# Kernel optimization log

Measured on AMD Instinct MI355X. Metric: run time of the kernel, lower is better.

Reference implementation:

```python
import jax, jax.numpy as jnp
import numpy as np

# dims: B=4 batch, S=2048 seq, D=4096 in, O=4096 out, E=16 adapters, R=16 rank

def setup_inputs() -> dict:
    key = jax.random.key(0)
    k = jax.random.split(key, 6)
    x = jax.random.normal(k[0], (4, 2048, 4096), jnp.float32)
    W = jax.random.normal(k[1], (4096, 4096), jnp.float32) * 0.02   # base_linear.weight [O, D]
    bias = jax.random.normal(k[2], (4096,), jnp.float32) * 0.02
    A = jax.random.normal(k[3], (16, 16, 4096), jnp.float32) * 0.02  # stacked a_factors [E, R, D]
    Bf = jax.random.normal(k[4], (16, 4096, 16), jnp.float32) * 0.02 # stacked b_factors [E, O, R]
    coeffs = jax.random.uniform(k[5], (16,), jnp.float32)            # task coefficients per adapter
    scales = jnp.full((16,), 0.5, jnp.float32)                       # per-adapter static scales
    return {"x": x, "W": W, "bias": bias, "A": A, "Bf": Bf, "coeffs": coeffs, "scales": scales}

def reference(x, W, bias, A, Bf, coeffs, scales):
    # base: out = x @ W.T + bias
    out = jnp.einsum('bsd,od->bso', x, W) + bias
    # fused LoRA: sum_e coeffs[e]*scales[e] * (x @ A[e].T) @ Bf[e].T
    xa = jnp.einsum('bsd,erd->ebsr', x, A)          # [E, B, S, R] (small: R=16)
    w = coeffs * scales                               # [E]
    upd = jnp.einsum('ebsr,eor,e->bso', xa, Bf, w)  # weighted accumulate over adapters
    return out + upd
```

## Files before the change

### kernel.cpp

```cpp
#include <hip/hip_runtime.h>

typedef float f32x4 __attribute__((ext_vector_type(4)));
typedef __bf16 bf16x8 __attribute__((ext_vector_type(8)));
typedef unsigned short u16x8 __attribute__((ext_vector_type(8)));

__device__ __forceinline__ unsigned short f2bf(float f) {
  union { float f; unsigned int u; } v; v.f = f;
  unsigned int u = v.u;
  unsigned int r = (u + 0x7FFFu + ((u >> 16) & 1u)) >> 16;
  return (unsigned short)r;
}

__global__ void k_cast_bf16(const float* __restrict__ in,
                            unsigned short* __restrict__ out, int n8) {
  int i = blockIdx.x * blockDim.x + threadIdx.x;
  if (i >= n8) return;
  const f32x4* p = (const f32x4*)in;
  f32x4 a = p[2 * i], b = p[2 * i + 1];
  u16x8 o;
  o[0] = f2bf(a[0]); o[1] = f2bf(a[1]); o[2] = f2bf(a[2]); o[3] = f2bf(a[3]);
  o[4] = f2bf(b[0]); o[5] = f2bf(b[1]); o[6] = f2bf(b[2]); o[7] = f2bf(b[3]);
  ((u16x8*)out)[i] = o;
}

__global__ void k_build_bw(const float* __restrict__ Bf,
                           const float* __restrict__ coeffs,
                           const float* __restrict__ scales,
                           unsigned short* __restrict__ bw) {
  int t = blockIdx.x * 256 + threadIdx.x;
  int o = t >> 8, k = t & 255, e = k >> 4, r = k & 15;
  float v = coeffs[e] * scales[e] * Bf[((size_t)e * 4096 + o) * 16 + r];
  bw[t] = f2bf(v);
}

__global__ void k_build_at(const float* __restrict__ A,
                           unsigned short* __restrict__ at) {
  __shared__ float tile[64][65];
  int kt = blockIdx.x * 64, dt = blockIdx.y * 64;
  int tx = threadIdx.x & 63, ty = threadIdx.x >> 6;
#pragma unroll
  for (int j = 0; j < 64; j += 4)
    tile[ty + j][tx] = A[(size_t)(kt + ty + j) * 4096 + dt + tx];
  __syncthreads();
#pragma unroll
  for (int j = 0; j < 64; j += 4)
    at[(size_t)(dt + ty + j) * 256 + kt + tx] = f2bf(tile[tx][ty + j]);
}

template <int M_, int N_, int K_>
__global__ __launch_bounds__(256) void k_gemm_prep(
    const unsigned short* __restrict__ Abuf,
    const unsigned short* __restrict__ Bbuf,
    const float* __restrict__ Wadd,
    unsigned short* __restrict__ outB) {
  constexpr int NBN = N_ / 128;
  constexpr int NWG = (M_ / 128) * NBN;
  const int bid = blockIdx.x;
  const int swz = (bid & 7) * (NWG / 8) + (bid >> 3);
  const int bm = swz / NBN, bn = swz % NBN;

  __shared__ unsigned short ldsA[128 * 64];
  __shared__ unsigned short ldsB[128 * 64];

  const int t = threadIdx.x, w = t >> 6, l = t & 63;
  const int wr = w >> 1, wc = w & 1;

  f32x4 acc[4][4] = {};
  const int m0 = bm * 128, n0 = bn * 128;
  const int srow = w * 8 + (l >> 3);
  const int scol = (l & 7) * 8;
  const unsigned short* gA = Abuf + (size_t)(m0 + srow) * K_ + scol;
  const unsigned short* gB = Bbuf + (size_t)(n0 + srow) * K_ + scol;

  for (int kt = 0; kt < K_; kt += 64) {
#pragma unroll
    for (int i = 0; i < 4; ++i) {
      __builtin_amdgcn_global_load_lds(
          (__attribute__((address_space(1))) void*)(gA + (size_t)i * 32 * K_ + kt),
          (__attribute__((address_space(3))) void*)(ldsA + i * 2048 + w * 512), 16, 0, 0);
      __builtin_amdgcn_global_load_lds(
          (__attribute__((address_space(1))) void*)(gB + (size_t)i * 32 * K_ + kt),
          (__attribute__((address_space(3))) void*)(ldsB + i * 2048 + w * 512), 16, 0, 0);
    }
    __syncthreads();
#pragma unroll
    for (int kk = 0; kk < 2; ++kk) {
      const int col = kk * 32 + (l >> 4) * 8;
      const int arow = wr * 64 + (l & 15);
      const int brow = wc * 64 + (l & 15);
      bf16x8 af[4], bfv[4];
#pragma unroll
      for (int mi = 0; mi < 4; ++mi)
        af[mi] = *(const bf16x8*)&ldsA[(arow + mi * 16) * 64 + col];
#pragma unroll
      for (int ni = 0; ni < 4; ++ni)
        bfv[ni] = *(const bf16x8*)&ldsB[(brow + ni * 16) * 64 + col];
#pragma unroll
      for (int mi = 0; mi < 4; ++mi)
#pragma unroll
        for (int ni = 0; ni < 4; ++ni)
          acc[mi][ni] = __builtin_amdgcn_mfma_f32_16x16x32_bf16(
              af[mi], bfv[ni], acc[mi][ni], 0, 0, 0);
    }
    __syncthreads();
  }

  const int mrow0 = m0 + wr * 64 + (l >> 4) * 4;
  const int ncol0 = n0 + wc * 64 + (l & 15);
#pragma unroll
  for (int mi = 0; mi < 4; ++mi)
#pragma unroll
    for (int r = 0; r < 4; ++r) {
      const int m = mrow0 + mi * 16 + r;
#pragma unroll
      for (int ni = 0; ni < 4; ++ni) {
        const int n = ncol0 + ni * 16;
        outB[(size_t)m * N_ + n] = f2bf(acc[mi][ni][r] + Wadd[(size_t)m * N_ + n]);
      }
    }
}

template <int M_, int N_, int K_>
__global__ __launch_bounds__(512, 2) void k_gemm256(
    const unsigned short* __restrict__ Abuf,
    const unsigned short* __restrict__ Bbuf,
    const float* __restrict__ bias,
    float* __restrict__ outF) {
  constexpr int NBN = N_ / 256;
  constexpr int NWG = (M_ / 256) * NBN;
  constexpr int NT = K_ / 32;
  static_assert(NWG % 8 == 0, "bijective xcd swizzle");
  static_assert(NT >= 4, "pipeline depth");

  const int bid = blockIdx.x;
  const int swz = (bid & 7) * (NWG / 8) + (bid >> 3);
  const int bm = swz / NBN, bn = swz % NBN;
  const int m0 = bm * 256, n0 = bn * 256;

  __shared__ __attribute__((aligned(128))) unsigned short lds[65536];
  char* ldsb = (char*)lds;

  const int tid = threadIdx.x, w = tid >> 6, l = tid & 63;
  const int wr = w >> 2, wc = w & 3;

  const int scol = ((l & 3) ^ ((l >> 3) & 3)) * 8;
  const unsigned short* gA = Abuf + (size_t)(m0 + w * 16 + (l >> 2)) * K_ + scol;
  const unsigned short* gB = Bbuf + (size_t)(n0 + w * 16 + (l >> 2)) * K_ + scol;
  const int dA = w * 1024;
  const int dB = 16384 + w * 1024;

  const int qp = ((l >> 4) ^ ((l >> 1) & 3)) * 16;
  const int raOff = (wr * 128 + (l & 15)) * 64 + qp;
  const int rbOff = 16384 + (wc * 64 + (l & 15)) * 64 + qp;

  f32x4 acc[8][4] = {};

#define STAGE_T(tt)                                                               \
  do {                                                                            \
    const int bb0_ = ((tt) & 3) << 15;                                            \
    const size_t ko_ = (size_t)(tt) * 32;                                         \
    _Pragma("unroll") for (int i_ = 0; i_ < 2; ++i_) {                            \
      __builtin_amdgcn_global_load_lds(                                           \
          (__attribute__((address_space(1))) void*)(gA + (size_t)i_ * 128 * K_ + ko_), \
          (__attribute__((address_space(3))) void*)(ldsb + bb0_ + i_ * 8192 + dA),     \
          16, 0, 0);                                                              \
      __builtin_amdgcn_global_load_lds(                                           \
          (__attribute__((address_space(1))) void*)(gB + (size_t)i_ * 128 * K_ + ko_), \
          (__attribute__((address_space(3))) void*)(ldsb + bb0_ + i_ * 8192 + dB),     \
          16, 0, 0);                                                              \
    }                                                                             \
  } while (0)

  STAGE_T(0); STAGE_T(1); STAGE_T(2);

  for (int t = 0; t < NT; ++t) {
    if (t + 2 < NT)      asm volatile("s_waitcnt vmcnt(8)" ::: "memory");
    else if (t + 1 < NT) asm volatile("s_waitcnt vmcnt(4)" ::: "memory");
    else                 asm volatile("s_waitcnt vmcnt(0)" ::: "memory");
    __builtin_amdgcn_s_barrier();

    const int bb0 = (t & 3) << 15;
    bf16x8 af[8], bv[4];
#pragma unroll
    for (int mi = 0; mi < 8; ++mi)
      af[mi] = *(const bf16x8*)(ldsb + bb0 + raOff + mi * 1024);
#pragma unroll
    for (int ni = 0; ni < 4; ++ni)
      bv[ni] = *(const bf16x8*)(ldsb + bb0 + rbOff + ni * 1024);

    if (t + 3 < NT) STAGE_T(t + 3);

    __builtin_amdgcn_s_setprio(1);
#pragma unroll
    for (int mi = 0; mi < 8; ++mi)
#pragma unroll
      for (int ni = 0; ni < 4; ++ni)
        acc[mi][ni] = __builtin_amdgcn_mfma_f32_16x16x32_bf16(
            af[mi], bv[ni], acc[mi][ni], 0, 0, 0);
    __builtin_amdgcn_s_setprio(0);
  }
#undef STAGE_T

#pragma unroll
  for (int ni = 0; ni < 4; ++ni) {
    const int n = n0 + wc * 64 + ni * 16 + (l & 15);
    const float bv2 = bias[n];
#pragma unroll
    for (int mi = 0; mi < 8; ++mi) {
      const int m = m0 + wr * 128 + mi * 16 + (l >> 4) * 4;
#pragma unroll
      for (int r = 0; r < 4; ++r)
        outF[(size_t)(m + r) * N_ + n] = acc[mi][ni][r] + bv2;
    }
  }
}

extern "C" void kernel_launch(void* const* d_in, const int* in_sizes, int n_in,
                              void* d_out, int out_size, void* d_ws, size_t ws_size,
                              hipStream_t stream) {
  const float* x      = (const float*)d_in[0];
  const float* W      = (const float*)d_in[1];
  const float* bias   = (const float*)d_in[2];
  const float* A      = (const float*)d_in[3];
  const float* Bf     = (const float*)d_in[4];
  const float* coeffs = (const float*)d_in[5];
  const float* scales = (const float*)d_in[6];
  float* out = (float*)d_out;

  char* ws = (char*)d_ws;
  unsigned short* xb   = (unsigned short*)(ws);
  unsigned short* weff = (unsigned short*)(ws + 67108864);
  unsigned short* bw   = (unsigned short*)(ws + 67108864 + 33554432);
  unsigned short* at   = (unsigned short*)(ws + 67108864 + 33554432 + 2097152);

  k_cast_bf16<<<16384, 256, 0, stream>>>(x, xb, (8192 * 4096) / 8);
  k_build_bw<<<4096, 256, 0, stream>>>(Bf, coeffs, scales, bw);
  k_build_at<<<dim3(4, 64), 256, 0, stream>>>(A, at);
  k_gemm_prep<4096, 4096, 256><<<1024, 256, 0, stream>>>(bw, at, W, weff);
  k_gemm256<8192, 4096, 4096><<<512, 512, 0, stream>>>(xb, weff, bias, out);
}
```

Before: 353.0 us.

## Switch main GEMM to 128x128 tiles with double-buffered LDS and grid-stride cast

Replaces the 256x256, 512-thread, 4-stage pipelined GEMM with a 128x128, 256-thread kernel using two LDS buffers and a barrier before each prefetch. The aim is more resident blocks per CU and lower LDS use, trading away per-tile data reuse and pipeline depth. The bf16 cast kernel is also made grid-stride with fewer blocks to cut launch overhead. The smaller tiles double global/L2 traffic per flop and add a barrier per K step.

```diff
diff --git a/kernel.cpp b/kernel.cpp
--- a/kernel.cpp
+++ b/kernel.cpp
@@ -11,16 +11,16 @@
   return (unsigned short)r;
 }
 
-__global__ void k_cast_bf16(const float* __restrict__ in,
-                            unsigned short* __restrict__ out, int n8) {
-  int i = blockIdx.x * blockDim.x + threadIdx.x;
-  if (i >= n8) return;
+__global__ __launch_bounds__(256) void k_cast_bf16(const float* __restrict__ in,
+                                                   unsigned short* __restrict__ out, int n8) {
   const f32x4* p = (const f32x4*)in;
-  f32x4 a = p[2 * i], b = p[2 * i + 1];
-  u16x8 o;
-  o[0] = f2bf(a[0]); o[1] = f2bf(a[1]); o[2] = f2bf(a[2]); o[3] = f2bf(a[3]);
-  o[4] = f2bf(b[0]); o[5] = f2bf(b[1]); o[6] = f2bf(b[2]); o[7] = f2bf(b[3]);
-  ((u16x8*)out)[i] = o;
+  for (int i = blockIdx.x * 256 + threadIdx.x; i < n8; i += 2048 * 256) {
+    f32x4 a = p[2 * i], b = p[2 * i + 1];
+    u16x8 o;
+    o[0] = f2bf(a[0]); o[1] = f2bf(a[1]); o[2] = f2bf(a[2]); o[3] = f2bf(a[3]);
+    o[4] = f2bf(b[0]); o[5] = f2bf(b[1]); o[6] = f2bf(b[2]); o[7] = f2bf(b[3]);
+    ((u16x8*)out)[i] = o;
+  }
 }
 
 __global__ void k_build_bw(const float* __restrict__ Bf,
@@ -121,83 +121,85 @@
 }
 
 template <int M_, int N_, int K_>
-__global__ __launch_bounds__(512, 2) void k_gemm256(
+__global__ __launch_bounds__(256, 4) void k_gemm128(
     const unsigned short* __restrict__ Abuf,
     const unsigned short* __restrict__ Bbuf,
     const float* __restrict__ bias,
     float* __restrict__ outF) {
-  constexpr int NBN = N_ / 256;
-  constexpr int NWG = (M_ / 256) * NBN;
+  constexpr int NBN = N_ / 128;
+  constexpr int NWG = (M_ / 128) * NBN;
   constexpr int NT = K_ / 32;
   static_assert(NWG % 8 == 0, "bijective xcd swizzle");
-  static_assert(NT >= 4, "pipeline depth");
+  static_assert(NT >= 2, "pipeline depth");
 
   const int bid = blockIdx.x;
   const int swz = (bid & 7) * (NWG / 8) + (bid >> 3);
   const int bm = swz / NBN, bn = swz % NBN;
-  const int m0 = bm * 256, n0 = bn * 256;
-
-  __shared__ __attribute__((aligned(128))) unsigned short lds[65536];
+  const int m0 = bm * 128, n0 = bn * 128;
+
+  __shared__ __attribute__((aligned(128))) unsigned short lds[16384];
   char* ldsb = (char*)lds;
 
   const int tid = threadIdx.x, w = tid >> 6, l = tid & 63;
-  const int wr = w >> 2, wc = w & 3;
+  const int wr = w >> 1, wc = w & 1;
 
   const int scol = ((l & 3) ^ ((l >> 3) & 3)) * 8;
   const unsigned short* gA = Abuf + (size_t)(m0 + w * 16 + (l >> 2)) * K_ + scol;
   const unsigned short* gB = Bbuf + (size_t)(n0 + w * 16 + (l >> 2)) * K_ + scol;
   const int dA = w * 1024;
-  const int dB = 16384 + w * 1024;
-
-  const int qp = ((l >> 4) ^ ((l >> 1) & 3)) * 16;
-  const int raOff = (wr * 128 + (l & 15)) * 64 + qp;
-  const int rbOff = 16384 + (wc * 64 + (l & 15)) * 64 + qp;
-
-  f32x4 acc[8][4] = {};
-
-#define STAGE_T(tt)                                                               \
-  do {                                                                            \
-    const int bb0_ = ((tt) & 3) << 15;                                            \
-    const size_t ko_ = (size_t)(tt) * 32;                                         \
-    _Pragma("unroll") for (int i_ = 0; i_ < 2; ++i_) {                            \
-      __builtin_amdgcn_global_load_lds(                                           \
-          (__attribute__((address_space(1))) void*)(gA + (size_t)i_ * 128 * K_ + ko_), \
-          (__attribute__((address_space(3))) void*)(ldsb + bb0_ + i_ * 8192 + dA),     \
-          16, 0, 0);                                                              \
-      __builtin_amdgcn_global_load_lds(                                           \
-          (__attribute__((address_space(1))) void*)(gB + (size_t)i_ * 128 * K_ + ko_), \
-          (__attribute__((address_space(3))) void*)(ldsb + bb0_ + i_ * 8192 + dB),     \
-          16, 0, 0);                                                              \
-    }                                                                             \
+  const int dB = 8192 + w * 1024;
+
+  const int qp = ((l >> 4) ^ ((l >> 1) & 3)) << 4;
+  const int raOff = wr * 4096 + (l & 15) * 64 + qp;
+  const int rbOff = 8192 + wc * 4096 + (l & 15) * 64 + qp;
+
+  f32x4 acc[4][4] = {};
+
+#define STAGE_T(tt)                                                                   \
+  do {                                                                                \
+    const int bb_ = ((tt) & 1) * 16384;                                               \
+    const size_t ko_ = (size_t)(tt) * 32;                                             \
+    _Pragma("unroll") for (int i_ = 0; i_ < 2; ++i_) {                                \
+      __builtin_amdgcn_global_load_lds(                                               \
+          (__attribute__((address_space(1))) void*)(gA + (size_t)i_ * 64 * K_ + ko_), \
+          (__attribute__((address_space(3))) void*)(ldsb + bb_ + i_ * 4096 + dA),     \
+          16, 0, 0);                                                                  \
+      __builtin_amdgcn_global_load_lds(                                               \
+          (__attribute__((address_space(1))) void*)(gB + (size_t)i_ * 64 * K_ + ko_), \
+          (__attribute__((address_space(3))) void*)(ldsb + bb_ + i_ * 4096 + dB),     \
+          16, 0, 0);                                                                  \
+    }                                                                                 \
   } while (0)
 
-  STAGE_T(0); STAGE_T(1); STAGE_T(2);
+  STAGE_T(0); STAGE_T(1);
 
   for (int t = 0; t < NT; ++t) {
-    if (t + 2 < NT)      asm volatile("s_waitcnt vmcnt(8)" ::: "memory");
-    else if (t + 1 < NT) asm volatile("s_waitcnt vmcnt(4)" ::: "memory");
-    else                 asm volatile("s_waitcnt vmcnt(0)" ::: "memory");
+    if (t + 1 < NT) asm volatile("s_waitcnt vmcnt(4)" ::: "memory");
+    else            asm volatile("s_waitcnt vmcnt(0)" ::: "memory");
     __builtin_amdgcn_s_barrier();
-
-    const int bb0 = (t & 3) << 15;
-    bf16x8 af[8], bv[4];
-#pragma unroll
-    for (int mi = 0; mi < 8; ++mi)
+    __builtin_amdgcn_sched_barrier(0);
+
+    const int bb0 = (t & 1) * 16384;
+    bf16x8 af[4], bv[4];
+#pragma unroll
+    for (int mi = 0; mi < 4; ++mi)
       af[mi] = *(const bf16x8*)(ldsb + bb0 + raOff + mi * 1024);
 #pragma unroll
     for (int ni = 0; ni < 4; ++ni)
       bv[ni] = *(const bf16x8*)(ldsb + bb0 + rbOff + ni * 1024);
 
-    if (t + 3 < NT) STAGE_T(t + 3);
-
     __builtin_amdgcn_s_setprio(1);
 #pragma unroll
-    for (int mi = 0; mi < 8; ++mi)
+    for (int mi = 0; mi < 4; ++mi)
 #pragma unroll
       for (int ni = 0; ni < 4; ++ni)
         acc[mi][ni] = __builtin_amdgcn_mfma_f32_16x16x32_bf16(
             af[mi], bv[ni], acc[mi][ni], 0, 0, 0);
     __builtin_amdgcn_s_setprio(0);
+
+    __builtin_amdgcn_s_barrier();
+    __builtin_amdgcn_sched_barrier(0);
+    if (t + 2 < NT) STAGE_T(t + 2);
   }
 #undef STAGE_T
 
@@ -206,8 +208,8 @@
     const int n = n0 + wc * 64 + ni * 16 + (l & 15);
     const float bv2 = bias[n];
 #pragma unroll
-    for (int mi = 0; mi < 8; ++mi) {
-      const int m = m0 + wr * 128 + mi * 16 + (l >> 4) * 4;
+    for (int mi = 0; mi < 4; ++mi) {
+      const int m = m0 + wr * 64 + mi * 16 + (l >> 4) * 4;
 #pragma unroll
       for (int r = 0; r < 4; ++r)
         outF[(size_t)(m + r) * N_ + n] = acc[mi][ni][r] + bv2;
@@ -233,9 +235,9 @@
   unsigned short* bw   = (unsigned short*)(ws + 67108864 + 33554432);
   unsigned short* at   = (unsigned short*)(ws + 67108864 + 33554432 + 2097152);
 
-  k_cast_bf16<<<16384, 256, 0, stream>>>(x, xb, (8192 * 4096) / 8);
+  k_cast_bf16<<<2048, 256, 0, stream>>>(x, xb, (8192 * 4096) / 8);
   k_build_bw<<<4096, 256, 0, stream>>>(Bf, coeffs, scales, bw);
   k_build_at<<<dim3(4, 64), 256, 0, stream>>>(A, at);
   k_gemm_prep<4096, 4096, 256><<<1024, 256, 0, stream>>>(bw, at, W, weff);
-  k_gemm256<8192, 4096, 4096><<<512, 512, 0, stream>>>(xb, weff, bias, out);
-}
+  k_gemm128<8192, 4096, 4096><<<2048, 256, 0, stream>>>(xb, weff, bias, out);
+}
```

Measured after the change: 465.9 us. 32.0% more time.

## Load GEMM B operand directly to registers and shrink LDS ring to A-only

Applied to the files above, without the earlier changes.

The main GEMM no longer stages the weight (B) operand through LDS. Each wave loads its B fragments straight into registers with inline global_load_dwordx4 into four rotating register sets. Only A goes through a 5-slot LDS ring, unrolled by four K-steps with two barriers per group instead of one per step. This cuts LDS footprint and LDS read traffic so occupancy can rise, at the cost of more VGPRs, redundant B global loads across the two wave rows, and hand-tuned vmcnt counts that are fragile. The cast kernel also becomes a grid-stride loop over 2048 blocks.

```diff
diff --git a/kernel.cpp b/kernel.cpp
--- a/kernel.cpp
+++ b/kernel.cpp
@@ -11,16 +11,16 @@
   return (unsigned short)r;
 }
 
-__global__ void k_cast_bf16(const float* __restrict__ in,
-                            unsigned short* __restrict__ out, int n8) {
-  int i = blockIdx.x * blockDim.x + threadIdx.x;
-  if (i >= n8) return;
+__global__ __launch_bounds__(256) void k_cast_bf16(const float* __restrict__ in,
+                                                   unsigned short* __restrict__ out, int n8) {
   const f32x4* p = (const f32x4*)in;
-  f32x4 a = p[2 * i], b = p[2 * i + 1];
-  u16x8 o;
-  o[0] = f2bf(a[0]); o[1] = f2bf(a[1]); o[2] = f2bf(a[2]); o[3] = f2bf(a[3]);
-  o[4] = f2bf(b[0]); o[5] = f2bf(b[1]); o[6] = f2bf(b[2]); o[7] = f2bf(b[3]);
-  ((u16x8*)out)[i] = o;
+  for (int i = blockIdx.x * 256 + threadIdx.x; i < n8; i += 2048 * 256) {
+    f32x4 a = p[2 * i], b = p[2 * i + 1];
+    u16x8 o;
+    o[0] = f2bf(a[0]); o[1] = f2bf(a[1]); o[2] = f2bf(a[2]); o[3] = f2bf(a[3]);
+    o[4] = f2bf(b[0]); o[5] = f2bf(b[1]); o[6] = f2bf(b[2]); o[7] = f2bf(b[3]);
+    ((u16x8*)out)[i] = o;
+  }
 }
 
 __global__ void k_build_bw(const float* __restrict__ Bf,
@@ -130,14 +130,14 @@
   constexpr int NWG = (M_ / 256) * NBN;
   constexpr int NT = K_ / 32;
   static_assert(NWG % 8 == 0, "bijective xcd swizzle");
-  static_assert(NT >= 4, "pipeline depth");
+  static_assert(NT % 4 == 0 && NT >= 8, "pipeline depth");
 
   const int bid = blockIdx.x;
   const int swz = (bid & 7) * (NWG / 8) + (bid >> 3);
   const int bm = swz / NBN, bn = swz % NBN;
   const int m0 = bm * 256, n0 = bn * 256;
 
-  __shared__ __attribute__((aligned(128))) unsigned short lds[65536];
+  __shared__ __attribute__((aligned(128))) unsigned short lds[40960];
   char* ldsb = (char*)lds;
 
   const int tid = threadIdx.x, w = tid >> 6, l = tid & 63;
@@ -145,61 +145,117 @@
 
   const int scol = ((l & 3) ^ ((l >> 3) & 3)) * 8;
   const unsigned short* gA = Abuf + (size_t)(m0 + w * 16 + (l >> 2)) * K_ + scol;
-  const unsigned short* gB = Bbuf + (size_t)(n0 + w * 16 + (l >> 2)) * K_ + scol;
   const int dA = w * 1024;
-  const int dB = 16384 + w * 1024;
-
-  const int qp = ((l >> 4) ^ ((l >> 1) & 3)) * 16;
+
+  const int qp = ((l >> 4) ^ ((l >> 1) & 3)) << 4;
   const int raOff = (wr * 128 + (l & 15)) * 64 + qp;
-  const int rbOff = 16384 + (wc * 64 + (l & 15)) * 64 + qp;
+
+  const unsigned long long bB0 =
+      (unsigned long long)(uintptr_t)Bbuf +
+      2ull * ((unsigned long long)(n0 + wc * 64 + (l & 15)) * K_ + ((l >> 4) * 8));
+  const unsigned long long niStep = (unsigned long long)16 * K_ * 2;
+  const unsigned long long bB1 = bB0 + niStep;
+  const unsigned long long bB2 = bB0 + 2 * niStep;
+  const unsigned long long bB3 = bB0 + 3 * niStep;
 
   f32x4 acc[8][4] = {};
-
-#define STAGE_T(tt)                                                               \
-  do {                                                                            \
-    const int bb0_ = ((tt) & 3) << 15;                                            \
-    const size_t ko_ = (size_t)(tt) * 32;                                         \
-    _Pragma("unroll") for (int i_ = 0; i_ < 2; ++i_) {                            \
-      __builtin_amdgcn_global_load_lds(                                           \
+  bf16x8 bs0[4], bs1[4], bs2[4], bs3[4];
+
+#define GLB(dst, base, toff)                                              \
+  asm volatile("global_load_dwordx4 %0, %1, off"                         \
+               : "=v"(dst)                                                \
+               : "v"((base) + (unsigned long long)(unsigned)(toff))       \
+               : "memory")
+#define LOADB(S, toff)                                                    \
+  do {                                                                    \
+    GLB(S[0], bB0, toff); GLB(S[1], bB1, toff);                           \
+    GLB(S[2], bB2, toff); GLB(S[3], bB3, toff);                           \
+  } while (0)
+
+#define STAGE_A(tt, bf)                                                                \
+  do {                                                                                 \
+    const int bb_ = (bf) * 16384;                                                      \
+    const size_t ko_ = (size_t)(tt) * 32;                                              \
+    _Pragma("unroll") for (int i_ = 0; i_ < 2; ++i_) {                                 \
+      __builtin_amdgcn_global_load_lds(                                                \
           (__attribute__((address_space(1))) void*)(gA + (size_t)i_ * 128 * K_ + ko_), \
-          (__attribute__((address_space(3))) void*)(ldsb + bb0_ + i_ * 8192 + dA),     \
-          16, 0, 0);                                                              \
-      __builtin_amdgcn_global_load_lds(                                           \
-          (__attribute__((address_space(1))) void*)(gB + (size_t)i_ * 128 * K_ + ko_), \
-          (__attribute__((address_space(3))) void*)(ldsb + bb0_ + i_ * 8192 + dB),     \
-          16, 0, 0);                                                              \
-    }                                                                             \
-  } while (0)
-
-  STAGE_T(0); STAGE_T(1); STAGE_T(2);
-
-  for (int t = 0; t < NT; ++t) {
-    if (t + 2 < NT)      asm volatile("s_waitcnt vmcnt(8)" ::: "memory");
-    else if (t + 1 < NT) asm volatile("s_waitcnt vmcnt(4)" ::: "memory");
-    else                 asm volatile("s_waitcnt vmcnt(0)" ::: "memory");
-    __builtin_amdgcn_s_barrier();
-
-    const int bb0 = (t & 3) << 15;
-    bf16x8 af[8], bv[4];
-#pragma unroll
-    for (int mi = 0; mi < 8; ++mi)
-      af[mi] = *(const bf16x8*)(ldsb + bb0 + raOff + mi * 1024);
-#pragma unroll
-    for (int ni = 0; ni < 4; ++ni)
-      bv[ni] = *(const bf16x8*)(ldsb + bb0 + rbOff + ni * 1024);
-
-    if (t + 3 < NT) STAGE_T(t + 3);
-
-    __builtin_amdgcn_s_setprio(1);
-#pragma unroll
-    for (int mi = 0; mi < 8; ++mi)
-#pragma unroll
-      for (int ni = 0; ni < 4; ++ni)
-        acc[mi][ni] = __builtin_amdgcn_mfma_f32_16x16x32_bf16(
-            af[mi], bv[ni], acc[mi][ni], 0, 0, 0);
-    __builtin_amdgcn_s_setprio(0);
-  }
-#undef STAGE_T
+          (__attribute__((address_space(3))) void*)(ldsb + bb_ + i_ * 8192 + dA),      \
+          16, 0, 0);                                                                   \
+    }                                                                                  \
+  } while (0)
+
+#define RD_A(mi, bf) (*(const bf16x8*)(ldsb + (bf) * 16384 + raOff + (mi) * 1024))
+
+#define TILE(bf, S)                                                                     \
+  do {                                                                                  \
+    bf16x8 fa0 = RD_A(0, bf), fa1 = RD_A(1, bf), fa2 = RD_A(2, bf), fa3 = RD_A(3, bf);  \
+    bf16x8 fa4 = RD_A(4, bf), fa5 = RD_A(5, bf), fa6 = RD_A(6, bf), fa7 = RD_A(7, bf);  \
+    __builtin_amdgcn_s_setprio(1);                                                      \
+    _Pragma("unroll") for (int ni_ = 0; ni_ < 4; ++ni_) {                               \
+      acc[0][ni_] = __builtin_amdgcn_mfma_f32_16x16x32_bf16(fa0, S[ni_], acc[0][ni_], 0, 0, 0); \
+      acc[1][ni_] = __builtin_amdgcn_mfma_f32_16x16x32_bf16(fa1, S[ni_], acc[1][ni_], 0, 0, 0); \
+      acc[2][ni_] = __builtin_amdgcn_mfma_f32_16x16x32_bf16(fa2, S[ni_], acc[2][ni_], 0, 0, 0); \
+      acc[3][ni_] = __builtin_amdgcn_mfma_f32_16x16x32_bf16(fa3, S[ni_], acc[3][ni_], 0, 0, 0); \
+      acc[4][ni_] = __builtin_amdgcn_mfma_f32_16x16x32_bf16(fa4, S[ni_], acc[4][ni_], 0, 0, 0); \
+      acc[5][ni_] = __builtin_amdgcn_mfma_f32_16x16x32_bf16(fa5, S[ni_], acc[5][ni_], 0, 0, 0); \
+      acc[6][ni_] = __builtin_amdgcn_mfma_f32_16x16x32_bf16(fa6, S[ni_], acc[6][ni_], 0, 0, 0); \
+      acc[7][ni_] = __builtin_amdgcn_mfma_f32_16x16x32_bf16(fa7, S[ni_], acc[7][ni_], 0, 0, 0); \
+    }                                                                                   \
+    __builtin_amdgcn_s_setprio(0);                                                      \
+  } while (0)
+
+#define TOPWAIT(n)                                                        \
+  do {                                                                    \
+    __builtin_amdgcn_sched_barrier(0);                                    \
+    asm volatile("s_waitcnt vmcnt(" #n ")" ::: "memory");                 \
+    __builtin_amdgcn_s_barrier();                                         \
+    __builtin_amdgcn_sched_barrier(0);                                    \
+  } while (0)
+
+  LOADB(bs0, 0);
+  LOADB(bs1, 64);
+  STAGE_A(0, 0);
+  STAGE_A(1, 1);
+  LOADB(bs2, 128);
+  STAGE_A(2, 2);
+  LOADB(bs3, 192);
+
+  int bT = 0;
+  for (int b = 0; b < NT / 4; ++b) {
+    const int T0 = 4 * b;
+    const int b1 = (bT + 1 >= 5) ? bT + 1 - 5 : bT + 1;
+    const int b2 = (bT + 2 >= 5) ? bT + 2 - 5 : bT + 2;
+    const int b3 = (bT + 3 >= 5) ? bT + 3 - 5 : bT + 3;
+    const int b4 = (bT + 4 >= 5) ? bT + 4 - 5 : bT + 4;
+
+    if (T0 == 0) TOPWAIT(10);
+    else         TOPWAIT(6);
+
+    TILE(bT, bs0);
+    if (T0 + 4 < NT) LOADB(bs0, (T0 + 4) * 64);
+    if (T0 + 3 < NT) STAGE_A(T0 + 3, b3);
+    TILE(b1, bs1);
+    if (T0 + 5 < NT) LOADB(bs1, (T0 + 5) * 64);
+    if (T0 + 4 < NT) STAGE_A(T0 + 4, b4);
+
+    if (T0 + 4 < NT) TOPWAIT(6);
+    else             TOPWAIT(0);
+
+    TILE(b2, bs2);
+    if (T0 + 6 < NT) LOADB(bs2, (T0 + 6) * 64);
+    if (T0 + 5 < NT) STAGE_A(T0 + 5, bT);
+    TILE(b3, bs3);
+    if (T0 + 7 < NT) LOADB(bs3, (T0 + 7) * 64);
+    if (T0 + 6 < NT) STAGE_A(T0 + 6, b1);
+
+    bT = (bT + 4 >= 5) ? bT + 4 - 5 : bT + 4;
+  }
+#undef GLB
+#undef LOADB
+#undef STAGE_A
+#undef RD_A
+#undef TILE
+#undef TOPWAIT
 
 #pragma unroll
   for (int ni = 0; ni < 4; ++ni) {
@@ -233,7 +289,7 @@
   unsigned short* bw   = (unsigned short*)(ws + 67108864 + 33554432);
   unsigned short* at   = (unsigned short*)(ws + 67108864 + 33554432 + 2097152);
 
-  k_cast_bf16<<<16384, 256, 0, stream>>>(x, xb, (8192 * 4096) / 8);
+  k_cast_bf16<<<2048, 256, 0, stream>>>(x, xb, (8192 * 4096) / 8);
   k_build_bw<<<4096, 256, 0, stream>>>(Bf, coeffs, scales, bw);
   k_build_at<<<dim3(4, 64), 256, 0, stream>>>(A, at);
   k_gemm_prep<4096, 4096, 256><<<1024, 256, 0, stream>>>(bw, at, W, weff);
```

Result: slower. 442.8 us (+25.5%).
